# Performance work log

Hardware: AMD Instinct MI355X
Metric: run time of the kernel (lower is better)

## Reference

```python
import math
import jax, jax.numpy as jnp
import numpy as np

B, T, N, D, H = 4, 12, 512, 256, 8


def _xavier(key, shape):
    limit = math.sqrt(6.0 / (shape[0] + shape[1]))
    return jax.random.uniform(key, shape, jnp.float32, -limit, limit)


def setup_inputs() -> dict:
    key = jax.random.key(0)
    kx, ks, kq, kk, kv, ko = jax.random.split(key, 6)
    return {
        "x": jax.random.normal(kx, (B, T, N, D), jnp.float32),
        "sim": jax.random.normal(ks, (N, N), jnp.float32),
        "Wq": _xavier(kq, (D, D)),
        "Wk": _xavier(kk, (D, D)),
        "Wv": _xavier(kv, (D, D)),
        "Wo": _xavier(ko, (D, D)),
    }


def reference(x, sim, Wq, Wk, Wv, Wo):
    # x: [B, T, N, D]; attention over spatial dim N, per (batch, time, head).
    b, t, n, d = x.shape
    hd = d // H
    scale = 1.0 / math.sqrt(hd)

    def split_heads(z):  # [B,T,N,D] -> [B,H,T,N,hd]
        return z.reshape(b, t, n, H, hd).transpose(0, 3, 1, 2, 4)

    q = split_heads(x @ Wq)
    k = split_heads(x @ Wk)
    v = split_heads(x @ Wv)

    # scores: [B,H,T,N,N]; additive sim bias broadcast over B,H,T
    scores = jnp.einsum("bhtnd,bhtmd->bhtnm", q, k) * scale + sim
    attn = jax.nn.softmax(scores, axis=-1)  # (dropout p=0.1 omitted: eval mode)
    out = jnp.einsum("bhtnm,bhtmd->bhtnd", attn, v)
    out = out.transpose(0, 2, 3, 1, 4).reshape(b, t, n, d)  # merge heads
    return out @ Wo
```

## Files before the change

kernel.cpp:

```cpp
#include <hip/hip_runtime.h>
#include <hip/hip_bf16.h>

#define BTT 48
#define SEQ 512
#define DIM 256
#define NH  8
#define HD  32
#define QKVD 768

typedef unsigned short u16;
typedef __attribute__((ext_vector_type(8))) short bf16x8;
typedef __attribute__((ext_vector_type(4))) float f32x4;

__device__ __forceinline__ float fexp2(float x) {
#if __has_builtin(__builtin_amdgcn_exp2f)
  return __builtin_amdgcn_exp2f(x);
#else
  float r; asm("v_exp_f32 %0, %1" : "=v"(r) : "v"(x)); return r;
#endif
}
__device__ __forceinline__ unsigned cvtpk_bf16(float lo, float hi) {
  unsigned r;
  asm("v_cvt_pk_bf16_f32 %0, %1, %2" : "=v"(r) : "v"(lo), "v"(hi));
  return r;
}

__device__ __forceinline__ u16 f2b(float f) {
  __hip_bfloat16 h = __float2bfloat16(f);
  union { __hip_bfloat16 h; u16 u; } c; c.h = h; return c.u;
}
__device__ __forceinline__ bf16x8 ldfrag8(const u16* p) {
  union { uint2 u[2]; bf16x8 v; } f;
  f.u[0] = *reinterpret_cast<const uint2*>(p);
  f.u[1] = *reinterpret_cast<const uint2*>(p + 4);
  return f.v;
}
__device__ __forceinline__ bf16x8 ldfrag16(const u16* p) {
  union { uint4 u; bf16x8 v; } f;
  f.u = *reinterpret_cast<const uint4*>(p);
  return f.v;
}

__global__ __launch_bounds__(256) void wtcvt4_kernel(const float* __restrict__ W0,
                                                     const float* __restrict__ W1,
                                                     const float* __restrict__ W2,
                                                     const float* __restrict__ W3,
                                                     u16* __restrict__ dst, float sc0) {
  __shared__ float Ls[64][65];
  const int z = blockIdx.z;
  const float* W = (z == 0) ? W0 : (z == 1) ? W1 : (z == 2) ? W2 : W3;
  u16* Bt = dst + (size_t)z * DIM * DIM;
  const float sc = (z == 0) ? sc0 : 1.0f;
  const int t = threadIdx.x;
  const int kt = blockIdx.x * 64, nt = blockIdx.y * 64;
#pragma unroll
  for (int it = 0; it < 4; ++it) {
    int r = (t >> 4) + it * 16;
    int c = (t & 15) * 4;
    float4 v = *reinterpret_cast<const float4*>(&W[(size_t)(kt + r) * 256 + nt + c]);
    Ls[r][c] = v.x; Ls[r][c + 1] = v.y; Ls[r][c + 2] = v.z; Ls[r][c + 3] = v.w;
  }
  __syncthreads();
  const int n = t >> 2, kc = (t & 3) * 16;
  union { uint4 u[2]; u16 s[16]; } ob;
#pragma unroll
  for (int j = 0; j < 16; ++j) ob.s[j] = f2b(Ls[kc + j][n] * sc);
  u16* dp = Bt + (size_t)(nt + n) * 256 + kt + kc;
  *reinterpret_cast<uint4*>(dp)     = ob.u[0];
  *reinterpret_cast<uint4*>(dp + 8) = ob.u[1];
}

__global__ __launch_bounds__(256) void simpack_kernel(const float* __restrict__ sim,
                                                      float* __restrict__ simT2) {
  const float LOG2E = 1.4426950408889634f;
  int gid = blockIdx.x * 256 + threadIdx.x;
  int q = gid & 511, k4 = gid >> 9;
  float4 v = *reinterpret_cast<const float4*>(&sim[(size_t)q * 512 + k4 * 4]);
  v.x *= LOG2E; v.y *= LOG2E; v.z *= LOG2E; v.w *= LOG2E;
  *reinterpret_cast<float4*>(&simT2[((size_t)k4 * 512 + q) * 4]) = v;
}

template <typename AIN, typename OUT>
__global__ __launch_bounds__(256) void gemm_mfma(const AIN* __restrict__ A,
                                                 const u16* __restrict__ Bt,
                                                 OUT* __restrict__ C,
                                                 int M, int N, int K) {
  __shared__ u16 As[128][36];
  __shared__ u16 Bs[128][36];
  const int t = threadIdx.x, lane = t & 63, w = t >> 6;
  const int g = lane >> 4, ln = lane & 15;
  const int bm = blockIdx.x * 128, bn = blockIdx.y * 128;
  const int wr = (w & 1) * 64, wc = (w >> 1) * 64;
  const f32x4 zf = {0.f, 0.f, 0.f, 0.f};
  f32x4 acc[4][4];
#pragma unroll
  for (int i = 0; i < 4; ++i)
#pragma unroll
    for (int j = 0; j < 4; ++j) acc[i][j] = zf;

  const int r0 = t >> 2, c8 = (t & 3) * 8;
  uint4 bpre[2];
  float4 apf0[2], apf1[2];
  uint4 apb[2];
#pragma unroll
  for (int p = 0; p < 2; ++p) {
    const size_t arow = (size_t)(bm + r0 + p * 64) * K + c8;
    if constexpr (sizeof(AIN) == 4) {
      apf0[p] = *reinterpret_cast<const float4*>((const float*)A + arow);
      apf1[p] = *reinterpret_cast<const float4*>((const float*)A + arow + 4);
    } else {
      apb[p] = *reinterpret_cast<const uint4*>((const u16*)A + arow);
    }
    bpre[p] = *reinterpret_cast<const uint4*>(&Bt[(size_t)(bn + r0 + p * 64) * K + c8]);
  }

  for (int k0 = 0; k0 < K; k0 += 32) {
#pragma unroll
    for (int p = 0; p < 2; ++p) {
      const int r = r0 + p * 64;
      uint2 a0, a1;
      if constexpr (sizeof(AIN) == 4) {
        a0.x = cvtpk_bf16(apf0[p].x, apf0[p].y);
        a0.y = cvtpk_bf16(apf0[p].z, apf0[p].w);
        a1.x = cvtpk_bf16(apf1[p].x, apf1[p].y);
        a1.y = cvtpk_bf16(apf1[p].z, apf1[p].w);
      } else {
        union { uint4 u4; uint2 u2[2]; } av; av.u4 = apb[p];
        a0 = av.u2[0]; a1 = av.u2[1];
      }
      union { uint4 u4; uint2 u2[2]; } bv; bv.u4 = bpre[p];
      *reinterpret_cast<uint2*>(&As[r][c8])     = a0;
      *reinterpret_cast<uint2*>(&As[r][c8 + 4]) = a1;
      *reinterpret_cast<uint2*>(&Bs[r][c8])     = bv.u2[0];
      *reinterpret_cast<uint2*>(&Bs[r][c8 + 4]) = bv.u2[1];
    }
    if (k0 + 32 < K) {
#pragma unroll
      for (int p = 0; p < 2; ++p) {
        const size_t arow = (size_t)(bm + r0 + p * 64) * K + k0 + 32 + c8;
        if constexpr (sizeof(AIN) == 4) {
          apf0[p] = *reinterpret_cast<const float4*>((const float*)A + arow);
          apf1[p] = *reinterpret_cast<const float4*>((const float*)A + arow + 4);
        } else {
          apb[p] = *reinterpret_cast<const uint4*>((const u16*)A + arow);
        }
        bpre[p] = *reinterpret_cast<const uint4*>(&Bt[(size_t)(bn + r0 + p * 64) * K + k0 + 32 + c8]);
      }
    }
    __syncthreads();
    bf16x8 af[4], bfr[4];
#pragma unroll
    for (int i = 0; i < 4; ++i) af[i]  = ldfrag8(&As[wr + i * 16 + ln][g * 8]);
#pragma unroll
    for (int j = 0; j < 4; ++j) bfr[j] = ldfrag8(&Bs[wc + j * 16 + ln][g * 8]);
#pragma unroll
    for (int i = 0; i < 4; ++i)
#pragma unroll
      for (int j = 0; j < 4; ++j)
        acc[i][j] = __builtin_amdgcn_mfma_f32_16x16x32_bf16(af[i], bfr[j], acc[i][j], 0, 0, 0);
    __syncthreads();
  }
#pragma unroll
  for (int i = 0; i < 4; ++i)
#pragma unroll
    for (int j = 0; j < 4; ++j)
#pragma unroll
      for (int r = 0; r < 4; ++r) {
        const int row = bm + wr + i * 16 + g * 4 + r;
        const int col = bn + wc + j * 16 + ln;
        if constexpr (sizeof(OUT) == 2)
          ((u16*)C)[(size_t)row * N + col] = f2b(acc[i][j][r]);
        else
          ((float*)C)[(size_t)row * N + col] = acc[i][j][r];
      }
}

__global__ __launch_bounds__(256) void attn_mfma8(const u16* __restrict__ QKV,
                                                  const float* __restrict__ simT2,
                                                  u16* __restrict__ O) {
  __shared__ u16 Ks[64][36];
  __shared__ u16 Vt[32][68];
  __shared__ u16 Pws[4][2][16][68];

  const int t = threadIdx.x;
  const int lane = t & 63, w = t >> 6;
  const int g = lane >> 4, ln = lane & 15;
  const int qb = blockIdx.x * 128;
  const int h = blockIdx.y, bt = blockIdx.z;
  const size_t base = (size_t)bt * SEQ * QKVD + (size_t)h * HD;
  const u16* Qp = QKV + base;
  const u16* Kp = QKV + base + 256;
  const u16* Vp = QKV + base + 512;
  const size_t baseo = (size_t)bt * SEQ * DIM + (size_t)h * HD;
  const int wq = qb + w * 32;

  bf16x8 qf[2];
#pragma unroll
  for (int qt = 0; qt < 2; ++qt)
    qf[qt] = ldfrag16(&Qp[(size_t)(wq + qt * 16 + ln) * QKVD + g * 8]);

  const f32x4 zf = {0.f, 0.f, 0.f, 0.f};
  f32x4 o[2][2];
  float lacc[2];
#pragma unroll
  for (int qt = 0; qt < 2; ++qt) { o[qt][0] = zf; o[qt][1] = zf; lacc[qt] = 0.f; }

  const float4* bq[2];
#pragma unroll
  for (int qt = 0; qt < 2; ++qt)
    bq[qt] = (const float4*)simT2 + ((size_t)g * 512 + (wq + qt * 16 + ln));

  const int sr = t >> 2, sc8 = (t & 3) * 8;
  uint4 kreg = *reinterpret_cast<const uint4*>(&Kp[(size_t)sr * QKVD + sc8]);
  uint4 vreg = *reinterpret_cast<const uint4*>(&Vp[(size_t)sr * QKVD + sc8]);

  for (int it = 0; it < 8; ++it) {
    {
      union { uint4 u4; uint2 u2[2]; u16 s[8]; } kv, vv;
      kv.u4 = kreg; vv.u4 = vreg;
      *reinterpret_cast<uint2*>(&Ks[sr][sc8])     = kv.u2[0];
      *reinterpret_cast<uint2*>(&Ks[sr][sc8 + 4]) = kv.u2[1];
#pragma unroll
      for (int e = 0; e < 8; ++e) Vt[sc8 + e][sr] = vv.s[e];
    }
    if (it < 7) {
      const size_t off = (size_t)(it + 1) * 64 * QKVD + (size_t)sr * QKVD + sc8;
      kreg = *reinterpret_cast<const uint4*>(&Kp[off]);
      vreg = *reinterpret_cast<const uint4*>(&Vp[off]);
    }
    __syncthreads();

    float4 bc[2][4];
#pragma unroll
    for (int qt = 0; qt < 2; ++qt)
#pragma unroll
      for (int kt = 0; kt < 4; ++kt)
        bc[qt][kt] = bq[qt][kt * 2048];

    bf16x8 kf[4];
#pragma unroll
    for (int kt = 0; kt < 4; ++kt) kf[kt] = ldfrag8(&Ks[kt * 16 + ln][g * 8]);
    bf16x8 vf[2][2];
#pragma unroll
    for (int hf = 0; hf < 2; ++hf)
#pragma unroll
      for (int ks = 0; ks < 2; ++ks)
        vf[hf][ks] = ldfrag8(&Vt[hf * 16 + ln][ks * 32 + g * 8]);

#pragma unroll
    for (int qt = 0; qt < 2; ++qt) {
      f32x4 s[4];
#pragma unroll
      for (int kt = 0; kt < 4; ++kt) {
        const float4 b4 = bc[qt][kt];
        f32x4 ci = {b4.x, b4.y, b4.z, b4.w};
        s[kt] = ci;
      }
      __builtin_amdgcn_s_setprio(1);
#pragma unroll
      for (int kt = 0; kt < 4; ++kt)
        s[kt] = __builtin_amdgcn_mfma_f32_16x16x32_bf16(kf[kt], qf[qt], s[kt], 0, 0, 0);
      __builtin_amdgcn_s_setprio(0);
      bf16x8 pfr[2];
      if (qt > 0) {
#pragma unroll
        for (int ks = 0; ks < 2; ++ks)
          pfr[ks] = ldfrag8(&Pws[w][0][ln][ks * 32 + g * 8]);
      }
      float lsum = 0.f;
#pragma unroll
      for (int kt = 0; kt < 4; ++kt) {
        const float e0 = fexp2(s[kt][0]);
        const float e1 = fexp2(s[kt][1]);
        const float e2 = fexp2(s[kt][2]);
        const float e3 = fexp2(s[kt][3]);
        lsum += (e0 + e1) + (e2 + e3);
        uint2 pw;
        pw.x = cvtpk_bf16(e0, e1);
        pw.y = cvtpk_bf16(e2, e3);
        *reinterpret_cast<uint2*>(&Pws[w][qt][ln][kt * 16 + g * 4]) = pw;
      }
      lacc[qt] += lsum;
      if (qt > 0) {
        __builtin_amdgcn_s_setprio(1);
#pragma unroll
        for (int ks = 0; ks < 2; ++ks)
#pragma unroll
          for (int hf = 0; hf < 2; ++hf)
            o[0][hf] = __builtin_amdgcn_mfma_f32_16x16x32_bf16(pfr[ks], vf[hf][ks], o[0][hf], 0, 0, 0);
        __builtin_amdgcn_s_setprio(0);
      }
    }
    {
      bf16x8 pfr[2];
#pragma unroll
      for (int ks = 0; ks < 2; ++ks)
        pfr[ks] = ldfrag8(&Pws[w][1][ln][ks * 32 + g * 8]);
      __builtin_amdgcn_s_setprio(1);
#pragma unroll
      for (int ks = 0; ks < 2; ++ks)
#pragma unroll
        for (int hf = 0; hf < 2; ++hf)
          o[1][hf] = __builtin_amdgcn_mfma_f32_16x16x32_bf16(pfr[ks], vf[hf][ks], o[1][hf], 0, 0, 0);
      __builtin_amdgcn_s_setprio(0);
    }
#pragma unroll
    for (int qt = 0; qt < 2; ++qt) bq[qt] += 16 * 512;
    __syncthreads();
  }

#pragma unroll
  for (int qt = 0; qt < 2; ++qt) {
    float l = lacc[qt];
    l += __shfl_xor(l, 16);
    l += __shfl_xor(l, 32);
    const float invl = 1.0f / l;
#pragma unroll
    for (int r = 0; r < 4; ++r) {
      const float il = __shfl(invl, g * 4 + r);
      const int qrow = wq + qt * 16 + g * 4 + r;
      O[baseo + (size_t)qrow * DIM + ln]      = f2b(o[qt][0][r] * il);
      O[baseo + (size_t)qrow * DIM + 16 + ln] = f2b(o[qt][1][r] * il);
    }
  }
}

extern "C" void kernel_launch(void* const* d_in, const int* in_sizes, int n_in,
                              void* d_out, int out_size, void* d_ws, size_t ws_size,
                              hipStream_t stream) {
  const float* x   = (const float*)d_in[0];
  const float* sim = (const float*)d_in[1];
  const float* Wq  = (const float*)d_in[2];
  const float* Wk  = (const float*)d_in[3];
  const float* Wv  = (const float*)d_in[4];
  const float* Wo  = (const float*)d_in[5];
  float* out = (float*)d_out;

  const int M = BTT * SEQ;
  const size_t sz = (size_t)M * DIM;
  const int WN = DIM * DIM;
  const float SCALE2 = 0.17677669529663687f * 1.4426950408889634f;

  u16* QKVw  = (u16*)d_ws;
  u16* Aw    = QKVw + (size_t)M * QKVD;
  u16* Wqkvb = Aw + sz;
  u16* Wob   = Wqkvb + (size_t)3 * WN;
  float* simT2 = (float*)(Wob + WN);

  wtcvt4_kernel<<<dim3(4, 4, 4), 256, 0, stream>>>(Wq, Wk, Wv, Wo, Wqkvb, SCALE2);
  simpack_kernel<<<256, 256, 0, stream>>>(sim, simT2);

  gemm_mfma<float, u16><<<dim3(M / 128, QKVD / 128), 256, 0, stream>>>(x, Wqkvb, QKVw, M, QKVD, DIM);

  attn_mfma8<<<dim3(4, NH, BTT), 256, 0, stream>>>(QKVw, simT2, Aw);

  gemm_mfma<u16, float><<<dim3(M / 128, DIM / 128), 256, 0, stream>>>(Aw, Wob, out, M, DIM, DIM);
}
```

Before: 89.19 us.

## Halve attention query tile per block and remap blocks across XCDs

The attention kernel now gives each wave one 16-row query tile instead of two, so each block covers 64 queries and the grid doubles to 3072 blocks. Block indices are remapped so that consecutive blocks on the same XCD (flat & 7) share the same (batch-time, head) group, which should improve L2 reuse of that group's K/V and bias data. Each block still loads the full K/V for its head, so global K/V traffic and shared-memory staging per query double. The software interleaving of the two query tiles' MFMAs is removed in exchange for more parallelism and lower register pressure.

```diff
diff --git a/kernel.cpp b/kernel.cpp
--- a/kernel.cpp
+++ b/kernel.cpp
@@ -175,40 +175,37 @@
       }
 }
 
-__global__ __launch_bounds__(256) void attn_mfma8(const u16* __restrict__ QKV,
+__global__ __launch_bounds__(256) void attn_mfma9(const u16* __restrict__ QKV,
                                                   const float* __restrict__ simT2,
                                                   u16* __restrict__ O) {
   __shared__ u16 Ks[64][36];
   __shared__ u16 Vt[32][68];
-  __shared__ u16 Pws[4][2][16][68];
+  __shared__ u16 Pws[4][16][68];
 
   const int t = threadIdx.x;
   const int lane = t & 63, w = t >> 6;
   const int g = lane >> 4, ln = lane & 15;
-  const int qb = blockIdx.x * 128;
-  const int h = blockIdx.y, bt = blockIdx.z;
+
+  const int flat = blockIdx.x + 8 * (blockIdx.y + 8 * (int)blockIdx.z);
+  const int work = (flat & 7) * 384 + (flat >> 3);
+  const int qb = work & 7;
+  const int grp = work >> 3;
+  const int h = grp & 7, bt = grp >> 3;
+
   const size_t base = (size_t)bt * SEQ * QKVD + (size_t)h * HD;
   const u16* Qp = QKV + base;
   const u16* Kp = QKV + base + 256;
   const u16* Vp = QKV + base + 512;
   const size_t baseo = (size_t)bt * SEQ * DIM + (size_t)h * HD;
-  const int wq = qb + w * 32;
-
-  bf16x8 qf[2];
-#pragma unroll
-  for (int qt = 0; qt < 2; ++qt)
-    qf[qt] = ldfrag16(&Qp[(size_t)(wq + qt * 16 + ln) * QKVD + g * 8]);
+  const int wq = qb * 64 + w * 16;
+
+  bf16x8 qf = ldfrag16(&Qp[(size_t)(wq + ln) * QKVD + g * 8]);
 
   const f32x4 zf = {0.f, 0.f, 0.f, 0.f};
-  f32x4 o[2][2];
-  float lacc[2];
-#pragma unroll
-  for (int qt = 0; qt < 2; ++qt) { o[qt][0] = zf; o[qt][1] = zf; lacc[qt] = 0.f; }
-
-  const float4* bq[2];
-#pragma unroll
-  for (int qt = 0; qt < 2; ++qt)
-    bq[qt] = (const float4*)simT2 + ((size_t)g * 512 + (wq + qt * 16 + ln));
+  f32x4 o0 = zf, o1 = zf;
+  float lacc = 0.f;
+
+  const float4* bq = (const float4*)simT2 + ((size_t)g * 512 + (wq + ln));
 
   const int sr = t >> 2, sc8 = (t & 3) * 8;
   uint4 kreg = *reinterpret_cast<const uint4*>(&Kp[(size_t)sr * QKVD + sc8]);
@@ -230,12 +227,14 @@
     }
     __syncthreads();
 
-    float4 bc[2][4];
-#pragma unroll
-    for (int qt = 0; qt < 2; ++qt)
-#pragma unroll
-      for (int kt = 0; kt < 4; ++kt)
-        bc[qt][kt] = bq[qt][kt * 2048];
+    f32x4 s[4];
+#pragma unroll
+    for (int kt = 0; kt < 4; ++kt) {
+      const float4 b4 = bq[kt * 2048];
+      f32x4 ci = {b4.x, b4.y, b4.z, b4.w};
+      s[kt] = ci;
+    }
+    bq += 16 * 512;
 
     bf16x8 kf[4];
 #pragma unroll
@@ -247,80 +246,54 @@
       for (int ks = 0; ks < 2; ++ks)
         vf[hf][ks] = ldfrag8(&Vt[hf * 16 + ln][ks * 32 + g * 8]);
 
-#pragma unroll
-    for (int qt = 0; qt < 2; ++qt) {
-      f32x4 s[4];
-#pragma unroll
-      for (int kt = 0; kt < 4; ++kt) {
-        const float4 b4 = bc[qt][kt];
-        f32x4 ci = {b4.x, b4.y, b4.z, b4.w};
-        s[kt] = ci;
-      }
-      __builtin_amdgcn_s_setprio(1);
-#pragma unroll
-      for (int kt = 0; kt < 4; ++kt)
-        s[kt] = __builtin_amdgcn_mfma_f32_16x16x32_bf16(kf[kt], qf[qt], s[kt], 0, 0, 0);
-      __builtin_amdgcn_s_setprio(0);
-      bf16x8 pfr[2];
-      if (qt > 0) {
-#pragma unroll
-        for (int ks = 0; ks < 2; ++ks)
-          pfr[ks] = ldfrag8(&Pws[w][0][ln][ks * 32 + g * 8]);
-      }
-      float lsum = 0.f;
-#pragma unroll
-      for (int kt = 0; kt < 4; ++kt) {
-        const float e0 = fexp2(s[kt][0]);
-        const float e1 = fexp2(s[kt][1]);
-        const float e2 = fexp2(s[kt][2]);
-        const float e3 = fexp2(s[kt][3]);
-        lsum += (e0 + e1) + (e2 + e3);
-        uint2 pw;
-        pw.x = cvtpk_bf16(e0, e1);
-        pw.y = cvtpk_bf16(e2, e3);
-        *reinterpret_cast<uint2*>(&Pws[w][qt][ln][kt * 16 + g * 4]) = pw;
-      }
-      lacc[qt] += lsum;
-      if (qt > 0) {
-        __builtin_amdgcn_s_setprio(1);
-#pragma unroll
-        for (int ks = 0; ks < 2; ++ks)
-#pragma unroll
-          for (int hf = 0; hf < 2; ++hf)
-            o[0][hf] = __builtin_amdgcn_mfma_f32_16x16x32_bf16(pfr[ks], vf[hf][ks], o[0][hf], 0, 0, 0);
-        __builtin_amdgcn_s_setprio(0);
-      }
-    }
+    __builtin_amdgcn_s_setprio(1);
+#pragma unroll
+    for (int kt = 0; kt < 4; ++kt)
+      s[kt] = __builtin_amdgcn_mfma_f32_16x16x32_bf16(kf[kt], qf, s[kt], 0, 0, 0);
+    __builtin_amdgcn_s_setprio(0);
+
+    float lsum = 0.f;
+#pragma unroll
+    for (int kt = 0; kt < 4; ++kt) {
+      const float e0 = fexp2(s[kt][0]);
+      const float e1 = fexp2(s[kt][1]);
+      const float e2 = fexp2(s[kt][2]);
+      const float e3 = fexp2(s[kt][3]);
+      lsum += (e0 + e1) + (e2 + e3);
+      uint2 pw;
+      pw.x = cvtpk_bf16(e0, e1);
+      pw.y = cvtpk_bf16(e2, e3);
+      *reinterpret_cast<uint2*>(&Pws[w][ln][kt * 16 + g * 4]) = pw;
+    }
+    lacc += lsum;
+
     {
       bf16x8 pfr[2];
 #pragma unroll
       for (int ks = 0; ks < 2; ++ks)
-        pfr[ks] = ldfrag8(&Pws[w][1][ln][ks * 32 + g * 8]);
+        pfr[ks] = ldfrag8(&Pws[w][ln][ks * 32 + g * 8]);
       __builtin_amdgcn_s_setprio(1);
 #pragma unroll
-      for (int ks = 0; ks < 2; ++ks)
-#pragma unroll
-        for (int hf = 0; hf < 2; ++hf)
-          o[1][hf] = __builtin_amdgcn_mfma_f32_16x16x32_bf16(pfr[ks], vf[hf][ks], o[1][hf], 0, 0, 0);
+      for (int ks = 0; ks < 2; ++ks) {
+        o0 = __builtin_amdgcn_mfma_f32_16x16x32_bf16(pfr[ks], vf[0][ks], o0, 0, 0, 0);
+        o1 = __builtin_amdgcn_mfma_f32_16x16x32_bf16(pfr[ks], vf[1][ks], o1, 0, 0, 0);
+      }
       __builtin_amdgcn_s_setprio(0);
     }
-#pragma unroll
-    for (int qt = 0; qt < 2; ++qt) bq[qt] += 16 * 512;
     __syncthreads();
   }
 
-#pragma unroll
-  for (int qt = 0; qt < 2; ++qt) {
-    float l = lacc[qt];
+  {
+    float l = lacc;
     l += __shfl_xor(l, 16);
     l += __shfl_xor(l, 32);
     const float invl = 1.0f / l;
 #pragma unroll
     for (int r = 0; r < 4; ++r) {
       const float il = __shfl(invl, g * 4 + r);
-      const int qrow = wq + qt * 16 + g * 4 + r;
-      O[baseo + (size_t)qrow * DIM + ln]      = f2b(o[qt][0][r] * il);
-      O[baseo + (size_t)qrow * DIM + 16 + ln] = f2b(o[qt][1][r] * il);
+      const int qrow = wq + g * 4 + r;
+      O[baseo + (size_t)qrow * DIM + ln]      = f2b(o0[r] * il);
+      O[baseo + (size_t)qrow * DIM + 16 + ln] = f2b(o1[r] * il);
     }
   }
 }
@@ -352,7 +325,7 @@
 
   gemm_mfma<float, u16><<<dim3(M / 128, QKVD / 128), 256, 0, stream>>>(x, Wqkvb, QKVw, M, QKVD, DIM);
 
-  attn_mfma8<<<dim3(4, NH, BTT), 256, 0, stream>>>(QKVw, simT2, Aw);
+  attn_mfma9<<<dim3(8, NH, BTT), 256, 0, stream>>>(QKVw, simT2, Aw);
 
   gemm_mfma<u16, float><<<dim3(M / 128, DIM / 128), 256, 0, stream>>>(Aw, Wob, out, M, DIM, DIM);
 }
```

After: 95.26 us. 1.07x slower.

## Store V row-major in LDS and read with transpose loads; remap blocks to XCDs

Applied to the files above, without the earlier changes.

V tiles are now stored to shared memory untransposed with a single 16-byte store per thread, replacing the eight scalar transposing stores. The MFMA B fragments are then read with ds_read_b64_tr_b16 hardware transpose loads. Block indices are also remapped so consecutive work items land on the same XCD, meant to improve L2 reuse of K/V across the four query blocks of a head. The change adds an explicit lgkmcnt wait and sched barrier, which may limit overlap.

```diff
diff --git a/kernel.cpp b/kernel.cpp
--- a/kernel.cpp
+++ b/kernel.cpp
@@ -11,6 +11,7 @@
 typedef unsigned short u16;
 typedef __attribute__((ext_vector_type(8))) short bf16x8;
 typedef __attribute__((ext_vector_type(4))) float f32x4;
+typedef __attribute__((ext_vector_type(2))) unsigned int u32x2;
 
 __device__ __forceinline__ float fexp2(float x) {
 #if __has_builtin(__builtin_amdgcn_exp2f)
@@ -175,24 +176,32 @@
       }
 }
 
-__global__ __launch_bounds__(256) void attn_mfma8(const u16* __restrict__ QKV,
-                                                  const float* __restrict__ simT2,
-                                                  u16* __restrict__ O) {
+#define TRRD(dst, base, OFFSTR) \
+  asm volatile("ds_read_b64_tr_b16 %0, %1 offset:" OFFSTR : "=v"(dst) : "v"(base))
+
+__global__ __launch_bounds__(256) void attn_mfma10(const u16* __restrict__ QKV,
+                                                   const float* __restrict__ simT2,
+                                                   u16* __restrict__ O) {
   __shared__ u16 Ks[64][36];
-  __shared__ u16 Vt[32][68];
+  __shared__ u16 Vn[2][64][16];
   __shared__ u16 Pws[4][2][16][68];
 
   const int t = threadIdx.x;
   const int lane = t & 63, w = t >> 6;
   const int g = lane >> 4, ln = lane & 15;
-  const int qb = blockIdx.x * 128;
-  const int h = blockIdx.y, bt = blockIdx.z;
+
+  const int flat = blockIdx.x + 4 * (blockIdx.y + 8 * (int)blockIdx.z);
+  const int work = (flat & 7) * 192 + (flat >> 3);
+  const int qb = work & 3;
+  const int grp = work >> 2;
+  const int h = grp & 7, bt = grp >> 3;
+
   const size_t base = (size_t)bt * SEQ * QKVD + (size_t)h * HD;
   const u16* Qp = QKV + base;
   const u16* Kp = QKV + base + 256;
   const u16* Vp = QKV + base + 512;
   const size_t baseo = (size_t)bt * SEQ * DIM + (size_t)h * HD;
-  const int wq = qb + w * 32;
+  const int wq = qb * 128 + w * 32;
 
   bf16x8 qf[2];
 #pragma unroll
@@ -214,14 +223,16 @@
   uint4 kreg = *reinterpret_cast<const uint4*>(&Kp[(size_t)sr * QKVD + sc8]);
   uint4 vreg = *reinterpret_cast<const uint4*>(&Vp[(size_t)sr * QKVD + sc8]);
 
+  const unsigned trbase = (unsigned)(unsigned long long)(&Vn[0][0][0])
+                        + (unsigned)(g * 256 + ln * 8);
+
   for (int it = 0; it < 8; ++it) {
     {
-      union { uint4 u4; uint2 u2[2]; u16 s[8]; } kv, vv;
-      kv.u4 = kreg; vv.u4 = vreg;
+      union { uint4 u4; uint2 u2[2]; } kv;
+      kv.u4 = kreg;
       *reinterpret_cast<uint2*>(&Ks[sr][sc8])     = kv.u2[0];
       *reinterpret_cast<uint2*>(&Ks[sr][sc8 + 4]) = kv.u2[1];
-#pragma unroll
-      for (int e = 0; e < 8; ++e) Vt[sc8 + e][sr] = vv.s[e];
+      *reinterpret_cast<uint4*>(&Vn[sc8 >> 4][sr][sc8 & 15]) = vreg;
     }
     if (it < 7) {
       const size_t off = (size_t)(it + 1) * 64 * QKVD + (size_t)sr * QKVD + sc8;
@@ -240,12 +251,22 @@
     bf16x8 kf[4];
 #pragma unroll
     for (int kt = 0; kt < 4; ++kt) kf[kt] = ldfrag8(&Ks[kt * 16 + ln][g * 8]);
+
     bf16x8 vf[2][2];
-#pragma unroll
-    for (int hf = 0; hf < 2; ++hf)
-#pragma unroll
-      for (int ks = 0; ks < 2; ++ks)
-        vf[hf][ks] = ldfrag8(&Vt[hf * 16 + ln][ks * 32 + g * 8]);
+    {
+      u32x2 r00a, r00b, r01a, r01b, r10a, r10b, r11a, r11b;
+      TRRD(r00a, trbase, "0");     TRRD(r00b, trbase, "128");
+      TRRD(r01a, trbase, "1024");  TRRD(r01b, trbase, "1152");
+      TRRD(r10a, trbase, "2048");  TRRD(r10b, trbase, "2176");
+      TRRD(r11a, trbase, "3072");  TRRD(r11b, trbase, "3200");
+      asm volatile("s_waitcnt lgkmcnt(0)" ::: "memory");
+      __builtin_amdgcn_sched_barrier(0);
+      union { u32x2 p[2]; bf16x8 v; } u;
+      u.p[0] = r00a; u.p[1] = r00b; vf[0][0] = u.v;
+      u.p[0] = r01a; u.p[1] = r01b; vf[0][1] = u.v;
+      u.p[0] = r10a; u.p[1] = r10b; vf[1][0] = u.v;
+      u.p[0] = r11a; u.p[1] = r11b; vf[1][1] = u.v;
+    }
 
 #pragma unroll
     for (int qt = 0; qt < 2; ++qt) {
@@ -352,7 +373,7 @@
 
   gemm_mfma<float, u16><<<dim3(M / 128, QKVD / 128), 256, 0, stream>>>(x, Wqkvb, QKVw, M, QKVD, DIM);
 
-  attn_mfma8<<<dim3(4, NH, BTT), 256, 0, stream>>>(QKVw, simT2, Aw);
+  attn_mfma10<<<dim3(4, NH, BTT), 256, 0, stream>>>(QKVw, simT2, Aw);
 
   gemm_mfma<u16, float><<<dim3(M / 128, DIM / 128), 256, 0, stream>>>(Aw, Wob, out, M, DIM, DIM);
 }
```

Result: faster. 80.87 us (-9.3%).
